# Kernel optimization log

Measured on AMD Instinct MI355X. Metric: run time of the kernel, lower is better.

Reference implementation:

```python
import jax, jax.numpy as jnp
import numpy as np

DIM = 512
NUM_ITEM = 2048
K = 10


def setup_inputs() -> dict:
    key = jax.random.key(0)
    k1, k2, k3 = jax.random.split(key, 3)
    input1 = jax.random.normal(k1, (16, DIM, 32, 32), dtype=jnp.float32)
    input2 = jax.random.normal(k2, (16, DIM, 32, 32), dtype=jnp.float32)
    stdv = 1.0 / np.sqrt(DIM)
    mempool = jax.random.uniform(k3, (NUM_ITEM, DIM), minval=-stdv, maxval=stdv, dtype=jnp.float32)
    return {"input1": input1, "input2": input2, "mempool": mempool}


def _memorize(x, mempool):
    # x: [B, C, H, W] with C == DIM
    B, C, H, W = x.shape
    q = jnp.transpose(x, (0, 2, 3, 1)).reshape(-1, C)      # [N, C]
    att = jax.nn.softmax(q @ mempool.T, axis=1)            # [N, num_item]
    val, idx = jax.lax.top_k(att, K)                       # [N, K]
    val = jax.nn.softmax(val, axis=1)                      # renormalize top-k
    # scatter(val into zeros) @ mempool == gather rows of mempool and combine
    out = jnp.einsum('nk,nkd->nd', val, mempool[idx])      # [N, C]
    return jnp.transpose(out.reshape(B, H, W, C), (0, 3, 1, 2))


def reference(input1, input2, mempool):
    return (_memorize(input1, mempool), _memorize(input2, mempool))
```

## Files before the change

### kernel.cpp

```cpp
#include <hip/hip_runtime.h>
#include <math.h>

typedef __attribute__((ext_vector_type(4))) float f4;
typedef __attribute__((ext_vector_type(8))) _Float16 f16x8;
typedef __attribute__((ext_vector_type(8))) short bf16x8;
typedef __attribute__((ext_vector_type(4))) unsigned short u16x4;
typedef unsigned int u32;
typedef unsigned short u16;

#define DIMC  512
#define NITEM 2048
#define TK    10
#define WSP   (NITEM * DIMC)

#define TPB    512
#define PXB    64
#define RIT    256
#define NRND   8
#define NSLICE 16

#define MP_B   0
#define MP_PL  16384
#define Q_B    49152
#define Q_PL   4096
#define SSTR   66
#define LDS_BYTES 67584
#define MV_F 0
#define MI_F 5120
#define MM_F 10240
#define MS_F 10752
#define WB_F 11264
#define IB_F 11904

#define KSWZ(i) (((i) ^ ((i) >> 2)) & 3)

union h16 { _Float16 h; u16 u; };

__device__ __forceinline__ u32 bf16_rne(float f) {
    u32 u = __float_as_uint(f);
    return (u + 0x7fffu + ((u >> 16) & 1u)) >> 16;
}

__device__ __forceinline__ void split3(float f, u16& ph, u16& pb, u16& pr) {
    h16 a; a.h = (_Float16)f;
    float f0 = (float)a.h;
    ph = a.u;
    pb = (u16)bf16_rne(f);
    pr = (u16)bf16_rne(f - f0);
}

__global__ __launch_bounds__(256)
void preconv_kernel(const float* __restrict__ mp, u16* __restrict__ ws)
{
    int idx = (blockIdx.x * 256 + threadIdx.x) * 4;
    int i  = idx >> 9;
    int k0 = idx & 511;
    f4 v = *(const f4*)(mp + (size_t)i * 512 + k0);
    int s  = k0 >> 5, kl = k0 & 31;
    int pos = s * 32 + ((kl >> 2) & 3) * 8 + (kl >> 4) * 4;
    u16x4 pH, pB, pR;
#pragma unroll
    for (int e = 0; e < 4; ++e) {
        u16 h, b, r; split3(v[e], h, b, r);
        pH[e] = h; pB[e] = b; pR[e] = r;
    }
    size_t base = (size_t)i * 512 + pos;
    *(u16x4*)(ws + 0 * WSP + base) = pH;
    *(u16x4*)(ws + 1 * WSP + base) = pB;
    *(u16x4*)(ws + 2 * WSP + base) = pR;
}

__global__ __launch_bounds__(TPB, 4)
void memorize_mfma(const float* __restrict__ x0, const float* __restrict__ x1,
                   const float* __restrict__ mp, const u16* __restrict__ ws,
                   float* __restrict__ out)
{
    extern __shared__ char ldsb[];
    float* ldsf = (float*)ldsb;

    const int t    = threadIdx.x;
    const int lane = t & 63;
    const int w    = t >> 6;
    const int blk  = blockIdx.x;
    const int img  = blk >> 4;
    const int n0   = (blk & 15) * PXB;
    const int b    = img & 15;

    const float* x  = (img < 16) ? x0 : x1;
    const float* xb = x + (size_t)b * (DIMC * 1024);
    float* ob = out + (img < 16 ? (size_t)0 : (size_t)16 * DIMC * 1024)
                    + (size_t)b * (DIMC * 1024);

    const int l15 = lane & 15;
    const int lh  = lane >> 4;
    const int ksw = lh ^ KSWZ(l15);

    const int qp = t & 63;
    const int g  = t >> 6;

    float tv[TK]; int tix[TK];
#pragma unroll
    for (int q = 0; q < TK; ++q) { tv[q] = -INFINITY; tix[q] = 0x7fffffff; }
    float rm = -INFINITY, rs = 0.0f;

    const int scl  = t & 31;
    const int spx  = (t >> 5) << 2;
    const int spos = (((scl >> 2) & 3) << 3) + ((scl >> 4) << 2) + (scl & 3);
    const int sslot = spos >> 3;
    const int soff  = (spos & 7) << 1;

    const int itq = lane >> 2;
    const int slo = lane & 3;
    const int ksrc = slo ^ KSWZ(itq);

    const char* qb = ldsb + Q_B + (l15 << 6) + (ksw << 4);
    const char* ab = ldsb + MP_B + (size_t)((w << 5) + l15) * 64 + (ksw << 4);

#pragma unroll 1
    for (int r = 0; r < NRND; ++r) {
        f4 acc[2][4];
#pragma unroll
        for (int mt = 0; mt < 2; ++mt)
#pragma unroll
            for (int nt = 0; nt < 4; ++nt) acc[mt][nt] = (f4){0.f, 0.f, 0.f, 0.f};

#pragma unroll 1
        for (int s = 0; s < NSLICE; ++s) {
            __syncthreads();

            {
#pragma unroll
                for (int p = 0; p < 3; ++p) {
#pragma unroll
                    for (int qg = 0; qg < 2; ++qg) {
                        int I = (w << 5) + (qg << 4);
                        const u16* src = ws + (size_t)p * WSP
                                       + (size_t)(r * RIT + I + itq) * 512
                                       + (s << 5) + (ksrc << 3);
                        char* dst = ldsb + MP_B + p * MP_PL + I * 64;
                        __builtin_amdgcn_global_load_lds(
                            (const __attribute__((address_space(1))) u32*)src,
                            (__attribute__((address_space(3))) u32*)dst, 16, 0, 0);
                    }
                }
            }

            {
                const float* src = xb + (size_t)((s << 5) + scl) * 1024 + n0 + spx;
                f4 v = *(const f4*)src;
#pragma unroll
                for (int e = 0; e < 4; ++e) {
                    int px = spx + e;
                    u16 h, bb, rr; split3(v[e], h, bb, rr);
                    int ro = Q_B + (px << 6) + (((sslot ^ KSWZ(px)) << 4) | soff);
                    *(u16*)(ldsb + ro)            = h;
                    *(u16*)(ldsb + ro + Q_PL)     = bb;
                    *(u16*)(ldsb + ro + 2 * Q_PL) = rr;
                }
            }
            __syncthreads();

            f16x8  bqH[4];
            bf16x8 bqB[4], bqR[4];
#pragma unroll
            for (int nt = 0; nt < 4; ++nt) {
                bqH[nt] = *(const f16x8*) (qb + 0 * Q_PL + nt * 1024);
                bqB[nt] = *(const bf16x8*)(qb + 1 * Q_PL + nt * 1024);
                bqR[nt] = *(const bf16x8*)(qb + 2 * Q_PL + nt * 1024);
            }

#pragma unroll
            for (int mt = 0; mt < 2; ++mt) {
                f16x8  aH = *(const f16x8*) (ab + 0 * MP_PL + mt * 1024);
                bf16x8 aB = *(const bf16x8*)(ab + 1 * MP_PL + mt * 1024);
                bf16x8 aR = *(const bf16x8*)(ab + 2 * MP_PL + mt * 1024);
#pragma unroll
                for (int nt = 0; nt < 4; ++nt) {
                    f4 c = acc[mt][nt];
                    c = __builtin_amdgcn_mfma_f32_16x16x32_f16 (aH, bqH[nt], c, 0, 0, 0);
                    c = __builtin_amdgcn_mfma_f32_16x16x32_bf16(aB, bqR[nt], c, 0, 0, 0);
                    c = __builtin_amdgcn_mfma_f32_16x16x32_bf16(aR, bqB[nt], c, 0, 0, 0);
                    acc[mt][nt] = c;
                }
            }
        }

        __syncthreads();
#pragma unroll
        for (int mt = 0; mt < 2; ++mt) {
#pragma unroll
            for (int nt = 0; nt < 4; ++nt) {
                int row = (w << 5) + (mt << 4) + (lh << 2);
                int col = (nt << 4) + l15;
                float* sp = ldsf + row * SSTR + col;
                sp[0 * SSTR] = acc[mt][nt][0];
                sp[1 * SSTR] = acc[mt][nt][1];
                sp[2 * SSTR] = acc[mt][nt][2];
                sp[3 * SSTR] = acc[mt][nt][3];
            }
        }
        __syncthreads();

        float mloc = rm;
#pragma unroll 4
        for (int jj = 0; jj < 32; ++jj) {
            int   il = (g << 5) + jj;
            float v  = ldsf[il * SSTR + qp];
            mloc = fmaxf(mloc, v);
            if (v > tv[TK - 1]) {
                int   id = r * RIT + il;
                float cv = v; int ci = id;
#pragma unroll
                for (int q = 0; q < TK; ++q) {
                    bool  gt = cv > tv[q];
                    float nv = gt ? tv[q]  : cv;
                    int   ni = gt ? tix[q] : ci;
                    tv[q]  = gt ? cv : tv[q];
                    tix[q] = gt ? ci : tix[q];
                    cv = nv; ci = ni;
                }
            }
        }
        rs *= __expf(rm - mloc);
        rm = mloc;
#pragma unroll 4
        for (int jj = 0; jj < 32; ++jj) {
            int   il = (g << 5) + jj;
            float v  = ldsf[il * SSTR + qp];
            rs += __expf(v - rm);
        }
    }

    __syncthreads();
    {
#pragma unroll
        for (int q = 0; q < TK; ++q) {
            ldsf[MV_F + (qp * 8 + g) * TK + q] = tv[q];
            ldsf[MI_F + (qp * 8 + g) * TK + q] = __int_as_float(tix[q]);
        }
        ldsf[MM_F + qp * 8 + g] = rm;
        ldsf[MS_F + qp * 8 + g] = rs;
    }
    __syncthreads();

    if (t < 64) {
        const int p = t;
        float gm[8], gs[8];
#pragma unroll
        for (int G = 0; G < 8; ++G) {
            gm[G] = ldsf[MM_F + p * 8 + G];
            gs[G] = ldsf[MS_F + p * 8 + G];
        }
        float mstar = gm[0];
#pragma unroll
        for (int G = 1; G < 8; ++G) mstar = fmaxf(mstar, gm[G]);
        float Z = 0.0f;
#pragma unroll
        for (int G = 0; G < 8; ++G) Z += gs[G] * __expf(gm[G] - mstar);

        int h0=0,h1=0,h2=0,h3=0,h4=0,h5=0,h6=0,h7=0;
        float ov[TK]; int oi[TK];
#pragma unroll
        for (int o = 0; o < TK; ++o) {
            float bv = -INFINITY; int bi = 0x7fffffff; int bg = 0;
#define SEL(G, HG)                                                               \
            {                                                                    \
                float v  = ldsf[MV_F + (p * 8 + G) * TK + (HG)];                 \
                int   id = __float_as_int(ldsf[MI_F + (p * 8 + G) * TK + (HG)]); \
                if (v > bv || (v == bv && id < bi)) { bv = v; bi = id; bg = G; } \
            }
            SEL(0, h0) SEL(1, h1) SEL(2, h2) SEL(3, h3)
            SEL(4, h4) SEL(5, h5) SEL(6, h6) SEL(7, h7)
#undef SEL
            ov[o] = bv; oi[o] = bi;
            h0 += (bg == 0); h1 += (bg == 1); h2 += (bg == 2); h3 += (bg == 3);
            h4 += (bg == 4); h5 += (bg == 5); h6 += (bg == 6); h7 += (bg == 7);
        }
        float pv[TK];
#pragma unroll
        for (int o = 0; o < TK; ++o) pv[o] = __expf(ov[o] - mstar) / Z;
        float pmax = pv[0];
        float wgt[TK]; float W = 0.0f;
#pragma unroll
        for (int o = 0; o < TK; ++o) { wgt[o] = __expf(pv[o] - pmax); W += wgt[o]; }
#pragma unroll
        for (int o = 0; o < TK; ++o) {
            ldsf[WB_F + p * TK + o] = wgt[o] / W;
            ldsf[IB_F + p * TK + o] = __int_as_float(oi[o]);
        }
    }
    __syncthreads();

    {
        const int ep = t & 63, cg = t >> 6;
        float wr[TK]; const float* rows[TK];
#pragma unroll
        for (int o = 0; o < TK; ++o) {
            wr[o]   = ldsf[WB_F + ep * TK + o];
            rows[o] = mp + (size_t)__float_as_int(ldsf[IB_F + ep * TK + o]) * DIMC;
        }
        float* obase = ob + n0 + ep;
#pragma unroll 4
        for (int cc = 0; cc < 16; ++cc) {
            int c = cg * 64 + cc * 4;
            f4 a = {0.0f, 0.0f, 0.0f, 0.0f};
#pragma unroll
            for (int o = 0; o < TK; ++o) {
                f4 rv = *(const f4*)(rows[o] + c);
#pragma unroll
                for (int z = 0; z < 4; ++z) a[z] = fmaf(wr[o], rv[z], a[z]);
            }
#pragma unroll
            for (int z = 0; z < 4; ++z) obase[(size_t)(c + z) * 1024] = a[z];
        }
    }
}

extern "C" void kernel_launch(void* const* d_in, const int* in_sizes, int n_in,
                              void* d_out, int out_size, void* d_ws, size_t ws_size,
                              hipStream_t stream) {
    const float* x0  = (const float*)d_in[0];
    const float* x1  = (const float*)d_in[1];
    const float* mpl = (const float*)d_in[2];
    float* out = (float*)d_out;
    u16* ws = (u16*)d_ws;

    preconv_kernel<<<dim3(1024), dim3(256), 0, stream>>>(mpl, ws);
    memorize_mfma<<<dim3(512), dim3(TPB), LDS_BYTES, stream>>>(x0, x1, mpl, ws, out);
}
```

Before: 558.5 us.

## Load mempool fragments directly from global into registers and double-buffer query LDS

The precomputed split-precision mempool is re-laid out so each wave can read its MFMA A-fragments straight from global memory into registers, replacing the global_load_lds staging into shared memory. The query tile is double-buffered in LDS so the next slice is staged while the current one is computed, which removes one barrier per slice. The wave-to-tile mapping changes to 4 item tiles by 2 pixel tiles per wave. This cuts LDS traffic and synchronisation, but adds global-load latency on the critical path and raises register pressure.

After: 579.5 us. +3.8%, slower.

```diff
diff --git a/kernel.cpp b/kernel.cpp
--- a/kernel.cpp
+++ b/kernel.cpp
@@ -19,9 +19,7 @@
 #define NRND   8
 #define NSLICE 16
 
-#define MP_B   0
-#define MP_PL  16384
-#define Q_B    49152
+#define QB_SZ  12288
 #define Q_PL   4096
 #define SSTR   66
 #define LDS_BYTES 67584
@@ -57,14 +55,15 @@
     int k0 = idx & 511;
     f4 v = *(const f4*)(mp + (size_t)i * 512 + k0);
     int s  = k0 >> 5, kl = k0 & 31;
-    int pos = s * 32 + ((kl >> 2) & 3) * 8 + (kl >> 4) * 4;
+    int lh = (kl >> 2) & 3, pair = kl >> 4;
     u16x4 pH, pB, pR;
 #pragma unroll
     for (int e = 0; e < 4; ++e) {
         u16 h, b, r; split3(v[e], h, b, r);
         pH[e] = h; pB[e] = b; pR[e] = r;
     }
-    size_t base = (size_t)i * 512 + pos;
+    size_t base = (size_t)(i >> 4) * 8192 + (size_t)s * 512
+                + (size_t)(lh * 16 + (i & 15)) * 8 + pair * 4;
     *(u16x4*)(ws + 0 * WSP + base) = pH;
     *(u16x4*)(ws + 1 * WSP + base) = pB;
     *(u16x4*)(ws + 2 * WSP + base) = pR;
@@ -94,6 +93,8 @@
     const int l15 = lane & 15;
     const int lh  = lane >> 4;
     const int ksw = lh ^ KSWZ(l15);
+    const int ig  = w >> 1;
+    const int pg  = w & 1;
 
     const int qp = t & 63;
     const int g  = t >> 6;
@@ -109,94 +110,92 @@
     const int sslot = spos >> 3;
     const int soff  = (spos & 7) << 1;
 
-    const int itq = lane >> 2;
-    const int slo = lane & 3;
-    const int ksrc = slo ^ KSWZ(itq);
-
-    const char* qb = ldsb + Q_B + (l15 << 6) + (ksw << 4);
-    const char* ab = ldsb + MP_B + (size_t)((w << 5) + l15) * 64 + (ksw << 4);
+    const u16* aw = ws + (size_t)lane * 8 + (size_t)(ig * 4) * 8192;
+
+    const int qfb = (pg << 11) + (l15 << 6) + (ksw << 4);
+
+#define STAGE_Q(S, BUF)                                                        \
+    {                                                                          \
+        const float* src = xb + (size_t)(((S) << 5) + scl) * 1024 + n0 + spx;  \
+        f4 v = *(const f4*)src;                                                \
+        _Pragma("unroll")                                                      \
+        for (int e = 0; e < 4; ++e) {                                          \
+            int px = spx + e;                                                  \
+            u16 h, bb, rr; split3(v[e], h, bb, rr);                            \
+            int ro = (BUF) * QB_SZ + (px << 6)                                 \
+                   + (((sslot ^ KSWZ(px)) << 4) | soff);                       \
+            *(u16*)(ldsb + ro)            = h;                                 \
+            *(u16*)(ldsb + ro + Q_PL)     = bb;                                \
+            *(u16*)(ldsb + ro + 2 * Q_PL) = rr;                                \
+        }                                                                      \
+    }
+
+#define ALOAD(IT, S)                                                           \
+    {                                                                          \
+        const u16* ap = ar + ((size_t)(IT) << 13) + ((S) << 9);                \
+        aH[IT] = *(const f16x8*) (ap + 0 * WSP);                               \
+        aB[IT] = *(const bf16x8*)(ap + 1 * WSP);                               \
+        aR[IT] = *(const bf16x8*)(ap + 2 * WSP);                               \
+    }
 
 #pragma unroll 1
     for (int r = 0; r < NRND; ++r) {
-        f4 acc[2][4];
-#pragma unroll
-        for (int mt = 0; mt < 2; ++mt)
-#pragma unroll
-            for (int nt = 0; nt < 4; ++nt) acc[mt][nt] = (f4){0.f, 0.f, 0.f, 0.f};
+        const u16* ar = aw + ((size_t)r << 17);
+        f4 acc[4][2];
+#pragma unroll
+        for (int it = 0; it < 4; ++it)
+#pragma unroll
+            for (int pt = 0; pt < 2; ++pt) acc[it][pt] = (f4){0.f, 0.f, 0.f, 0.f};
+
+        __syncthreads();
+        STAGE_Q(0, 0)
+        __syncthreads();
 
 #pragma unroll 1
         for (int s = 0; s < NSLICE; ++s) {
+            const int cur = s & 1;
+
+            f16x8 aH[4]; bf16x8 aB[4], aR[4];
+            ALOAD(0, s)
+            ALOAD(1, s)
+
+            if (s + 1 < NSLICE) STAGE_Q(s + 1, cur ^ 1)
+
+            const char* qc = ldsb + cur * QB_SZ + qfb;
+            f16x8 qH[2]; bf16x8 qB[2], qR[2];
+#pragma unroll
+            for (int pt = 0; pt < 2; ++pt) {
+                qH[pt] = *(const f16x8*) (qc + 0 * Q_PL + pt * 1024);
+                qB[pt] = *(const bf16x8*)(qc + 1 * Q_PL + pt * 1024);
+                qR[pt] = *(const bf16x8*)(qc + 2 * Q_PL + pt * 1024);
+            }
+
+#pragma unroll
+            for (int it = 0; it < 4; ++it) {
+                if (it < 2) ALOAD(it + 2, s)
+#pragma unroll
+                for (int pt = 0; pt < 2; ++pt) {
+                    f4 c = acc[it][pt];
+                    c = __builtin_amdgcn_mfma_f32_16x16x32_f16 (aH[it], qH[pt], c, 0, 0, 0);
+                    c = __builtin_amdgcn_mfma_f32_16x16x32_bf16(aB[it], qR[pt], c, 0, 0, 0);
+                    c = __builtin_amdgcn_mfma_f32_16x16x32_bf16(aR[it], qB[pt], c, 0, 0, 0);
+                    acc[it][pt] = c;
+                }
+            }
             __syncthreads();
-
-            {
-#pragma unroll
-                for (int p = 0; p < 3; ++p) {
-#pragma unroll
-                    for (int qg = 0; qg < 2; ++qg) {
-                        int I = (w << 5) + (qg << 4);
-                        const u16* src = ws + (size_t)p * WSP
-                                       + (size_t)(r * RIT + I + itq) * 512
-                                       + (s << 5) + (ksrc << 3);
-                        char* dst = ldsb + MP_B + p * MP_PL + I * 64;
-                        __builtin_amdgcn_global_load_lds(
-                            (const __attribute__((address_space(1))) u32*)src,
-                            (__attribute__((address_space(3))) u32*)dst, 16, 0, 0);
-                    }
-                }
-            }
-
-            {
-                const float* src = xb + (size_t)((s << 5) + scl) * 1024 + n0 + spx;
-                f4 v = *(const f4*)src;
-#pragma unroll
-                for (int e = 0; e < 4; ++e) {
-                    int px = spx + e;
-                    u16 h, bb, rr; split3(v[e], h, bb, rr);
-                    int ro = Q_B + (px << 6) + (((sslot ^ KSWZ(px)) << 4) | soff);
-                    *(u16*)(ldsb + ro)            = h;
-                    *(u16*)(ldsb + ro + Q_PL)     = bb;
-                    *(u16*)(ldsb + ro + 2 * Q_PL) = rr;
-                }
-            }
-            __syncthreads();
-
-            f16x8  bqH[4];
-            bf16x8 bqB[4], bqR[4];
-#pragma unroll
-            for (int nt = 0; nt < 4; ++nt) {
-                bqH[nt] = *(const f16x8*) (qb + 0 * Q_PL + nt * 1024);
-                bqB[nt] = *(const bf16x8*)(qb + 1 * Q_PL + nt * 1024);
-                bqR[nt] = *(const bf16x8*)(qb + 2 * Q_PL + nt * 1024);
-            }
-
-#pragma unroll
-            for (int mt = 0; mt < 2; ++mt) {
-                f16x8  aH = *(const f16x8*) (ab + 0 * MP_PL + mt * 1024);
-                bf16x8 aB = *(const bf16x8*)(ab + 1 * MP_PL + mt * 1024);
-                bf16x8 aR = *(const bf16x8*)(ab + 2 * MP_PL + mt * 1024);
-#pragma unroll
-                for (int nt = 0; nt < 4; ++nt) {
-                    f4 c = acc[mt][nt];
-                    c = __builtin_amdgcn_mfma_f32_16x16x32_f16 (aH, bqH[nt], c, 0, 0, 0);
-                    c = __builtin_amdgcn_mfma_f32_16x16x32_bf16(aB, bqR[nt], c, 0, 0, 0);
-                    c = __builtin_amdgcn_mfma_f32_16x16x32_bf16(aR, bqB[nt], c, 0, 0, 0);
-                    acc[mt][nt] = c;
-                }
-            }
-        }
-
-        __syncthreads();
-#pragma unroll
-        for (int mt = 0; mt < 2; ++mt) {
-#pragma unroll
-            for (int nt = 0; nt < 4; ++nt) {
-                int row = (w << 5) + (mt << 4) + (lh << 2);
-                int col = (nt << 4) + l15;
+        }
+
+#pragma unroll
+        for (int it = 0; it < 4; ++it) {
+#pragma unroll
+            for (int pt = 0; pt < 2; ++pt) {
+                int row = (ig << 6) + (it << 4) + (lh << 2);
+                int col = (pg << 5) + (pt << 4) + l15;
                 float* sp = ldsf + row * SSTR + col;
-                sp[0 * SSTR] = acc[mt][nt][0];
-                sp[1 * SSTR] = acc[mt][nt][1];
-                sp[2 * SSTR] = acc[mt][nt][2];
-                sp[3 * SSTR] = acc[mt][nt][3];
+                sp[0 * SSTR] = acc[it][pt][0];
+                sp[1 * SSTR] = acc[it][pt][1];
+                sp[2 * SSTR] = acc[it][pt][2];
+                sp[3 * SSTR] = acc[it][pt][3];
             }
         }
         __syncthreads();
@@ -314,6 +313,8 @@
             for (int z = 0; z < 4; ++z) obase[(size_t)(c + z) * 1024] = a[z];
         }
     }
+#undef STAGE_Q
+#undef ALOAD
 }
 
 extern "C" void kernel_launch(void* const* d_in, const int* in_sizes, int n_in,
```
